# Optimization experiments

Measured on AMD Instinct MI355X. Metric: run time of the kernel, lower is better.

The kernel has to match this reference:

```python
import jax, jax.numpy as jnp
import numpy as np

B, S, D = 4, 2048, 1024

def setup_inputs() -> dict:
    key = jax.random.key(0)
    k1, k2, k3, k4 = jax.random.split(key, 4)
    scale = 1.0 / np.sqrt(D)  # roughly glorot-like magnitude for weights
    return {
        "inputs": jax.random.normal(k1, (B, S, D), dtype=jnp.float32),
        "W_query": jax.random.normal(k2, (D, D), dtype=jnp.float32) * scale,
        "W_key": jax.random.normal(k3, (D, D), dtype=jnp.float32) * scale,
        "W_value": jax.random.normal(k4, (D, D), dtype=jnp.float32) * scale,
    }

def reference(inputs, W_query, W_key, W_value):
    # QKV projections: [B,S,D] @ [D,D]
    q = jnp.einsum('bsd,de->bse', inputs, W_query)
    k = jnp.einsum('bsd,de->bse', inputs, W_key)
    v = jnp.einsum('bsd,de->bse', inputs, W_value)
    # Unscaled attention scores [B,S,S] (source applies no 1/sqrt(d))
    score = jnp.einsum('bqd,bkd->bqk', q, k)
    weights = jax.nn.softmax(score, axis=-1)
    context = jnp.einsum('bqk,bkd->bqd', weights, v)
    return context
```

## Files before the change

### kernel.cpp

```cpp
#include <hip/hip_runtime.h>
#include <math.h>


typedef __bf16 bf16;
typedef _Float16 f16;
typedef __bf16 bf16x8 __attribute__((ext_vector_type(8)));
typedef __bf16 bf16x4 __attribute__((ext_vector_type(4)));
typedef _Float16 f16x4 __attribute__((ext_vector_type(4)));
typedef _Float16 f16x8 __attribute__((ext_vector_type(8)));
typedef float  f32x4  __attribute__((ext_vector_type(4)));

template<typename E> struct vec8_of;
template<> struct vec8_of<bf16> { using type = bf16x8; };
template<> struct vec8_of<f16>  { using type = f16x8; };

__device__ inline f32x4 mfma16(bf16x8 a, bf16x8 b, f32x4 c) {
    return __builtin_amdgcn_mfma_f32_16x16x32_bf16(a, b, c, 0, 0, 0);
}
__device__ inline f32x4 mfma16(f16x8 a, f16x8 b, f32x4 c) {
    return __builtin_amdgcn_mfma_f32_16x16x32_f16(a, b, c, 0, 0, 0);
}

#define AS1 __attribute__((address_space(1)))
#define AS3 __attribute__((address_space(3)))

template<typename E>
__device__ inline void async_load16(const E* g, void* l) {
    __builtin_amdgcn_global_load_lds((const AS1 unsigned int*)g,
                                     (AS3 unsigned int*)l, 16, 0, 0);
}

#define SBAR()  do { __builtin_amdgcn_s_barrier(); __builtin_amdgcn_sched_barrier(0); } while (0)
#define WAITV(n) do { asm volatile("s_waitcnt vmcnt(" #n ")" ::: "memory"); __builtin_amdgcn_sched_barrier(0); } while (0)
#define WAITL() do { asm volatile("s_waitcnt lgkmcnt(0)" ::: "memory"); __builtin_amdgcn_sched_barrier(0); } while (0)

__device__ inline void xcd_swz(int nwg, int gx, int& bx, int& by) {
    const int flat = by * gx + bx;
    const int s = (flat & 7) * (nwg >> 3) + (flat >> 3);
    bx = s % gx;
    by = s / gx;
}

template<int OUT_MODE, int BMQ>
__device__ __forceinline__ void gemm8_body(
    char* __restrict__ smraw,
    const f16* __restrict__ A, const f16* __restrict__ B,
    float* __restrict__ Cf, f16* __restrict__ Ch,
    int K, int lda, int ldb, int ldc,
    long long sA, long long sB, long long sC,
    int bx, int by, int bz)
{
    constexpr int B0OFF = BMQ * 8192;
    constexpr int B1OFF = B0OFF + 8192;
    constexpr int BUFSZ = B0OFF + 16384;

    A += (long long)bz * sA;
    B += (long long)bz * sB;

    const int tid  = threadIdx.x;
    const int lane = tid & 63;
    const int wave = tid >> 6;
    const int quad = lane >> 4;
    const int l16  = lane & 15;
    const int wm   = wave >> 2;
    const int wn   = wave & 3;

    const long long rowA0 = (long long)by * (BMQ * 128);
    const long long colB0 = (long long)bx * 256;

    const int line0 = tid >> 3;
    const int slog  = (tid & 7) ^ (line0 & 7);
    const int aRow0 = line0 * 2 + (slog >> 2);
    const int aCol0 = (slog & 3) * 8;
    const int bRow  = ((aRow0 >> 5) << 6) + (aRow0 & 31);

    const f16* aSrc0 = A + (rowA0 + aRow0) * lda + aCol0;
    const f16* aSrc1 = A + (rowA0 + 128 + aRow0) * lda + aCol0;
    const f16* b0Src = B + (colB0 + bRow) * ldb + aCol0;
    const f16* b1Src = b0Src + 32LL * ldb;

    const int dA0 = tid * 16, dA1 = 8192 + tid * 16;

    const int nt = K >> 5;

    auto stageA = [&](int t) {
        char* buf = smraw + (t & 1) * BUFSZ;
        async_load16(aSrc0 + t * 32, buf + dA0);
        if (BMQ == 2) async_load16(aSrc1 + t * 32, buf + dA1);
    };
    auto stageB0 = [&](int t) {
        char* buf = smraw + (t & 1) * BUFSZ;
        async_load16(b0Src + t * 32, buf + B0OFF + dA0);
    };
    auto stageB1 = [&](int t) {
        char* buf = smraw + (t & 1) * BUFSZ;
        async_load16(b1Src + t * 32, buf + B1OFF + dA0);
    };

    const int h    = l16 >> 1;
    const int lofs = h * 128 + ((((l16 & 1) * 4 + quad) ^ h) << 4);
    const int aoff = wm * (BMQ * 4096) + lofs;
    const int boff = wn * 2048 + lofs;

    f32x4 acc[4 * BMQ][4];
#pragma unroll
    for (int i = 0; i < 4 * BMQ; i++)
#pragma unroll
        for (int j = 0; j < 4; j++) acc[i][j] = (f32x4){0.f, 0.f, 0.f, 0.f};

    stageA(0); stageB0(0); stageB1(0);
    stageA(1); stageB0(1);
    if constexpr (BMQ == 2) WAITV(4); else WAITV(3);
    SBAR();

    for (int t = 0; t < nt; t++) {
        const char* buf = smraw + (t & 1) * BUFSZ;
        f16x8 av[4 * BMQ], bv[2];

#pragma unroll
        for (int i = 0; i < 4 * BMQ; i++) av[i] = *(const f16x8*)(buf + aoff + i * 1024);
#pragma unroll
        for (int j = 0; j < 2; j++) bv[j] = *(const f16x8*)(buf + B0OFF + boff + j * 1024);
        if (t + 1 < nt) stageB1(t + 1);
        SBAR();
        WAITL();
        __builtin_amdgcn_s_setprio(1);
#pragma unroll
        for (int i = 0; i < 4 * BMQ; i++) {
            acc[i][0] = mfma16(av[i], bv[0], acc[i][0]);
            acc[i][1] = mfma16(av[i], bv[1], acc[i][1]);
        }
        __builtin_amdgcn_s_setprio(0);
        if (t + 1 < nt) { if constexpr (BMQ == 2) WAITV(4); else WAITV(3); }
        else WAITV(0);
        SBAR();

#pragma unroll
        for (int j = 0; j < 2; j++) bv[j] = *(const f16x8*)(buf + B1OFF + boff + j * 1024);
        if (t + 2 < nt) { stageA(t + 2); stageB0(t + 2); }
        SBAR();
        WAITL();
        __builtin_amdgcn_s_setprio(1);
#pragma unroll
        for (int i = 0; i < 4 * BMQ; i++) {
            acc[i][2] = mfma16(av[i], bv[0], acc[i][2]);
            acc[i][3] = mfma16(av[i], bv[1], acc[i][3]);
        }
        __builtin_amdgcn_s_setprio(0);
        if (t + 2 < nt) { if constexpr (BMQ == 2) WAITV(4); else WAITV(3); }
        else if (t + 1 < nt) WAITV(1);
        SBAR();
    }

    if constexpr (OUT_MODE == 2) {
        auto tr = (f16(*)[72])smraw;
        const int batch = (int)(rowA0 >> 11);
        const long long rib = rowA0 & 2047;
        const int c  = tid >> 1;
        const int r0 = (tid & 1) << 5;
#pragma unroll
        for (int h2 = 0; h2 < 2; h2++)
#pragma unroll
            for (int iq = 0; iq < 2; iq++) {
                __syncthreads();
                if (wm == h2) {
#pragma unroll
                    for (int i2 = 0; i2 < 4; i2++)
#pragma unroll
                        for (int j = 0; j < 4; j++)
#pragma unroll
                            for (int e = 0; e < 4; e++)
                                tr[wn * 64 + j * 16 + l16][i2 * 16 + quad * 4 + e] =
                                    (f16)acc[iq * 4 + i2][j][e];
                }
                __syncthreads();
                f16* vt = Ch + (long long)batch * 1024 * 2048 +
                          (long long)(colB0 + c) * ldc + rib + h2 * 128 + iq * 64 + r0;
#pragma unroll
                for (int u = 0; u < 32; u += 8)
                    *(f16x8*)(vt + u) = *(const f16x8*)&tr[c][r0 + u];
            }
        return;
    }

    const long long cOff = (long long)bz * sC +
                           (rowA0 + wm * (BMQ * 64) + quad * 4) * (long long)ldc +
                           colB0 + wn * 64 + l16;
#pragma unroll
    for (int i = 0; i < 4 * BMQ; i++)
#pragma unroll
        for (int e = 0; e < 4; e++) {
            const long long ro = cOff + (long long)(i * 16 + e) * ldc;
            if (OUT_MODE == 0) {
                float* rp = Cf + ro;
#pragma unroll
                for (int j = 0; j < 4; j++) rp[j * 16] = acc[i][j][e];
            } else {
                f16* rp = Ch + ro;
#pragma unroll
                for (int j = 0; j < 4; j++) rp[j * 16] = (f16)acc[i][j][e];
            }
        }
}

__global__ __launch_bounds__(512, 2) void tv8(
    const f16* __restrict__ Xf, const f16* __restrict__ Mt_f,
    const f16* __restrict__ Wvt_f, f16* __restrict__ T, f16* __restrict__ Vt)
{
    extern __shared__ char smraw[];
    int bx = blockIdx.x, by = blockIdx.y;
    xcd_swz(256, 8, bx, by);
    if (bx < 4)
        gemm8_body<1, 2>(smraw, Xf, Mt_f, nullptr, T, 1024, 1024, 1024, 1024,
                         0, 0, 0, bx, by, 0);
    else
        gemm8_body<2, 2>(smraw, Xf, Wvt_f, nullptr, Vt, 1024, 1024, 1024, 2048,
                         0, 0, 0, bx - 4, by, 0);
}

template<int OUT_MODE, int BMQ>
__global__ __launch_bounds__(512, 2) void gemm8_k(
    const f16* __restrict__ A, const f16* __restrict__ B,
    float* __restrict__ Cf, f16* __restrict__ Ch,
    int K, int lda, int ldb, int ldc,
    long long sA, long long sB, long long sC)
{
    extern __shared__ char smraw[];
    int bx = blockIdx.x, by = blockIdx.y;
    xcd_swz(gridDim.x * gridDim.y, gridDim.x, bx, by);
    gemm8_body<OUT_MODE, BMQ>(smraw, A, B, Cf, Ch, K, lda, ldb, ldc, sA, sB, sC,
                              bx, by, blockIdx.z);
}

template<typename E, bool SPLIT, int OUT_MODE, int BK>
__device__ __forceinline__ void gemm_body(
    char* __restrict__ smraw,
    const E* __restrict__ Ahi, const E* __restrict__ Alo,
    const E* __restrict__ Bhi, const E* __restrict__ Blo,
    float* __restrict__ Cf, f16* __restrict__ Ch,
    int K, int lda, int ldb, int ldc,
    long long sA, long long sB, long long sC,
    int bx, int by, int bz)
{
    using vec8 = typename vec8_of<E>::type;
    constexpr int TILE_BYTES = 128 * BK * (int)sizeof(E);
    constexpr int CPW = (TILE_BYTES / 1024) / 4;
    constexpr int SPR = (BK * (int)sizeof(E)) / 16;

    Ahi += (long long)bz * sA;
    Bhi += (long long)bz * sB;
    if (SPLIT) { Alo += (long long)bz * sA; Blo += (long long)bz * sB; }

    const int tid  = threadIdx.x;
    const int lane = tid & 63;
    const int wave = tid >> 6;
    const int quad = lane >> 4;
    const int l16  = lane & 15;
    const int wm   = (wave >> 1) * 64;
    const int wn   = (wave & 1) * 64;

    const long long rowA0 = (long long)by * 128;
    const long long colB0 = (long long)bx * 128;

    auto swz = [](int r) -> int { return (SPR == 8) ? (r & 7) : ((r >> 1) & 3); };

    int ofs[CPW], rr[CPW], cc8[CPW];
#pragma unroll
    for (int u = 0; u < CPW; u++) {
        ofs[u] = (wave * CPW + u) * 1024 + lane * 16;
        const int s = ofs[u] >> 4;
        rr[u]  = s / SPR;
        cc8[u] = (s & (SPR - 1)) ^ swz(rr[u]);
    }

    f32x4 acc[4][4];
#pragma unroll
    for (int i = 0; i < 4; i++)
#pragma unroll
        for (int j = 0; j < 4; j++) acc[i][j] = (f32x4){0.f, 0.f, 0.f, 0.f};

    for (int k0 = 0; k0 < K; k0 += BK) {
#pragma unroll
        for (int u = 0; u < CPW; u++) {
            async_load16(Ahi + (rowA0 + rr[u]) * lda + k0 + cc8[u] * 8, smraw + 0 * TILE_BYTES + ofs[u]);
            async_load16(Bhi + (colB0 + rr[u]) * ldb + k0 + cc8[u] * 8, smraw + 1 * TILE_BYTES + ofs[u]);
            if (SPLIT) {
                async_load16(Alo + (rowA0 + rr[u]) * lda + k0 + cc8[u] * 8, smraw + 2 * TILE_BYTES + ofs[u]);
                async_load16(Blo + (colB0 + rr[u]) * ldb + k0 + cc8[u] * 8, smraw + 3 * TILE_BYTES + ofs[u]);
            }
        }
        __syncthreads();

#pragma unroll
        for (int kh = 0; kh < BK / 32; kh++) {
            const int kc8 = kh * 4 + quad;
            vec8 a_hi[4], b_hi[4], a_lo[4], b_lo[4];
#pragma unroll
            for (int i = 0; i < 4; i++) {
                const int ra = wm + i * 16 + l16;
                const int rb = wn + i * 16 + l16;
                const int oa = ra * (SPR * 16) + ((kc8 ^ swz(ra)) << 4);
                const int ob = rb * (SPR * 16) + ((kc8 ^ swz(rb)) << 4);
                a_hi[i] = *(const vec8*)(smraw + 0 * TILE_BYTES + oa);
                b_hi[i] = *(const vec8*)(smraw + 1 * TILE_BYTES + ob);
                if (SPLIT) {
                    a_lo[i] = *(const vec8*)(smraw + 2 * TILE_BYTES + oa);
                    b_lo[i] = *(const vec8*)(smraw + 3 * TILE_BYTES + ob);
                }
            }
#pragma unroll
            for (int i = 0; i < 4; i++)
#pragma unroll
                for (int j = 0; j < 4; j++) {
                    acc[i][j] = mfma16(a_hi[i], b_hi[j], acc[i][j]);
                    if (SPLIT) {
                        acc[i][j] = mfma16(a_hi[i], b_lo[j], acc[i][j]);
                        acc[i][j] = mfma16(a_lo[i], b_hi[j], acc[i][j]);
                    }
                }
        }
        __syncthreads();
    }

    const long long cOff = (long long)bz * sC +
                           (rowA0 + wm + quad * 4) * (long long)ldc + colB0 + wn + l16;
#pragma unroll
    for (int i = 0; i < 4; i++)
#pragma unroll
        for (int e = 0; e < 4; e++) {
            const long long ro = cOff + (i * 16 + e) * ldc;
            if (OUT_MODE == 0) {
                float* rp = Cf + ro;
#pragma unroll
                for (int j = 0; j < 4; j++) rp[j * 16] = acc[i][j][e];
            } else {
                f16* rp = Ch + ro;
#pragma unroll
                for (int j = 0; j < 4; j++) rp[j * 16] = (f16)acc[i][j][e];
            }
        }
}

template<typename E, bool SPLIT, int OUT_MODE, int BK>
__global__ __launch_bounds__(256) void gemm_bt(
    const E* __restrict__ Ahi, const E* __restrict__ Alo,
    const E* __restrict__ Bhi, const E* __restrict__ Blo,
    float* __restrict__ Cf, f16* __restrict__ Ch,
    int K, int lda, int ldb, int ldc,
    long long sA, long long sB, long long sC)
{
    extern __shared__ char smraw[];
    gemm_body<E, SPLIT, OUT_MODE, BK>(smraw, Ahi, Alo, Bhi, Blo, Cf, Ch,
                                      K, lda, ldb, ldc, sA, sB, sC,
                                      blockIdx.x, blockIdx.y, blockIdx.z);
}

__global__ __launch_bounds__(256) void prep_all(
    const float4* __restrict__ X, f16* __restrict__ Xf,
    const float* __restrict__ Wq, const float* __restrict__ Wk, const float* __restrict__ Wv,
    bf16* __restrict__ Wq_h, bf16* __restrict__ Wq_l,
    bf16* __restrict__ Wk_h, bf16* __restrict__ Wk_l,
    f16* __restrict__ Wvt_f)
{
    int b = blockIdx.x;
    if (b < 8192) {
        long long i = (long long)b * 256 + threadIdx.x;
        float4 v = X[i];
        f16x4 fv = {(f16)v.x, (f16)v.y, (f16)v.z, (f16)v.w};
        *(f16x4*)(Xf + 4 * i) = fv;
    } else if (b < 10240) {
        const int b2 = b - 8192;
        const float4* W = (const float4*)(b2 < 1024 ? Wq : Wk);
        bf16* hh = b2 < 1024 ? Wq_h : Wk_h;
        bf16* ll = b2 < 1024 ? Wq_l : Wk_l;
        long long i = (long long)(b2 & 1023) * 256 + threadIdx.x;
        float4 v = W[i];
        bf16 a0 = (bf16)v.x, a1 = (bf16)v.y, a2 = (bf16)v.z, a3 = (bf16)v.w;
        bf16x4 hv = {a0, a1, a2, a3};
        bf16x4 lv = {(bf16)(v.x - (float)a0), (bf16)(v.y - (float)a1),
                     (bf16)(v.z - (float)a2), (bf16)(v.w - (float)a3)};
        *(bf16x4*)(hh + 4 * i) = hv;
        *(bf16x4*)(ll + 4 * i) = lv;
    } else {
        const int b3 = b - 10240;
        __shared__ float t[32][33];
        const int bx = (b3 & 31) * 32, by = (b3 >> 5) * 32;
        const int tx = threadIdx.x & 31, ty = threadIdx.x >> 5;
#pragma unroll
        for (int i = 0; i < 32; i += 8)
            t[ty + i][tx] = Wv[(long long)(by + ty + i) * 1024 + bx + tx];
        __syncthreads();
#pragma unroll
        for (int i = 0; i < 32; i += 8) {
            long long o = (long long)(bx + ty + i) * 1024 + by + tx;
            Wvt_f[o] = (f16)t[tx][ty + i];
        }
    }
}

__global__ __launch_bounds__(256) void softmax_f16(const float* __restrict__ S,
                                                   f16* __restrict__ P, int n)
{
    const long long row = blockIdx.x;
    const float4* p = (const float4*)(S + row * (long long)n);
    f16* q = P + row * (long long)n;
    const int tid = threadIdx.x;
    const int wv = tid >> 6, lane = tid & 63;

    float4 va = p[tid], vb = p[tid + 256];
    float v[8] = {va.x, va.y, va.z, va.w, vb.x, vb.y, vb.z, vb.w};
    float m = -3.4e38f;
#pragma unroll
    for (int i = 0; i < 8; i++) m = fmaxf(m, v[i]);
#pragma unroll
    for (int off = 32; off > 0; off >>= 1) m = fmaxf(m, __shfl_xor(m, off, 64));

    __shared__ float red[4];
    if (lane == 0) red[wv] = m;
    __syncthreads();
    m = fmaxf(fmaxf(red[0], red[1]), fmaxf(red[2], red[3]));

    float s = 0.f;
#pragma unroll
    for (int i = 0; i < 8; i++) { v[i] = __expf(v[i] - m); s += v[i]; }
#pragma unroll
    for (int off = 32; off > 0; off >>= 1) s += __shfl_xor(s, off, 64);
    __syncthreads();
    if (lane == 0) red[wv] = s;
    __syncthreads();
    s = red[0] + red[1] + red[2] + red[3];

    const float inv = 1.0f / s;
    f16x4 o0 = {(f16)(v[0] * inv), (f16)(v[1] * inv), (f16)(v[2] * inv), (f16)(v[3] * inv)};
    f16x4 o1 = {(f16)(v[4] * inv), (f16)(v[5] * inv), (f16)(v[6] * inv), (f16)(v[7] * inv)};
    *(f16x4*)(q + tid * 4) = o0;
    *(f16x4*)(q + 1024 + tid * 4) = o1;
}

extern "C" void kernel_launch(void* const* d_in, const int* in_sizes, int n_in,
                              void* d_out, int out_size, void* d_ws, size_t ws_size,
                              hipStream_t stream) {
    const float* X  = (const float*)d_in[0];
    const float* Wq = (const float*)d_in[1];
    const float* Wk = (const float*)d_in[2];
    const float* Wv = (const float*)d_in[3];
    float* out = (float*)d_out;

    char* w = (char*)d_ws;
    const long long MB = 1024LL * 1024;
    f16*  Xf    = (f16*) (w + 0 * MB);
    bf16* Wq_h  = (bf16*)(w + 16 * MB);
    bf16* Wq_l  = (bf16*)(w + 18 * MB);
    bf16* Wk_h  = (bf16*)(w + 20 * MB);
    bf16* Wk_l  = (bf16*)(w + 22 * MB);
    f16*  Wvt_f = (f16*) (w + 24 * MB);
    f16*  Mt_f  = (f16*) (w + 26 * MB);
    f16*  T     = (f16*) (w + 28 * MB);
    f16*  Vt    = (f16*) (w + 44 * MB);
    float* Sc   = (float*)(w + 60 * MB);
    f16*  P     = (f16*) (w + 124 * MB);

    dim3 blk(256);

    prep_all<<<dim3(11264), blk, 0, stream>>>(
        (const float4*)X, Xf, Wq, Wk, Wv, Wq_h, Wq_l, Wk_h, Wk_l, Wvt_f);

    gemm_bt<bf16, true, 1, 32><<<dim3(8, 8, 1), blk, 32768, stream>>>(
        Wk_h, Wk_l, Wq_h, Wq_l, nullptr, Mt_f,
        1024, 1024, 1024, 1024, 0, 0, 0);

    tv8<<<dim3(8, 32), dim3(512), 65536, stream>>>(Xf, Mt_f, Wvt_f, T, Vt);

    gemm8_k<0, 2><<<dim3(8, 8, 4), dim3(512), 65536, stream>>>(
        T, Xf, Sc, nullptr, 1024, 1024, 1024, 2048,
        2048LL * 1024, 2048LL * 1024, 2048LL * 2048);

    softmax_f16<<<dim3(4 * 2048), blk, 0, stream>>>(Sc, P, 2048);

    gemm8_k<0, 1><<<dim3(4, 16, 4), dim3(512), 49152, stream>>>(
        P, Vt, out, nullptr, 2048, 2048, 2048, 1024,
        2048LL * 2048, 1024LL * 2048, 2048LL * 1024);
}
```

Baseline: 273.3 us.

## Add deep-K double-buffered GEMM variant with 64-wide K stages for main GEMMs

Adds a new GEMM body that stages 64 K-elements per iteration (two 32-wide halves) into double-buffered LDS, splitting A and B loads across sub-phases so global loads overlap the MFMA work. Launches use 128KB/96KB of dynamic shared memory, with a fallback to the old kernels if the attribute cannot be set. It targets fewer barriers and loop iterations per K and better latency hiding, at the cost of LDS capacity and possibly fewer resident blocks per CU.

```diff
diff --git a/kernel.cpp b/kernel.cpp
--- a/kernel.cpp
+++ b/kernel.cpp
@@ -39,6 +39,220 @@
     const int s = (flat & 7) * (nwg >> 3) + (flat >> 3);
     bx = s % gx;
     by = s / gx;
+}
+
+template<int OUT_MODE, int BMQ>
+__device__ __forceinline__ void gemm_deep_body(
+    char* __restrict__ smraw,
+    const f16* __restrict__ A, const f16* __restrict__ B,
+    float* __restrict__ Cf, f16* __restrict__ Ch,
+    int K, int lda, int ldb, int ldc,
+    long long sA, long long sB, long long sC,
+    int bx, int by, int bz)
+{
+    constexpr int ACH   = BMQ * 8192;
+    constexpr int BOFF  = 2 * ACH;
+    constexpr int BUFSZ = 2 * ACH + 32768;
+    constexpr int nI    = 4 * BMQ;
+
+    A += (long long)bz * sA;
+    B += (long long)bz * sB;
+
+    const int tid  = threadIdx.x;
+    const int lane = tid & 63;
+    const int wave = tid >> 6;
+    const int quad = lane >> 4;
+    const int l16  = lane & 15;
+    const int wm   = wave >> 2;
+    const int wn   = wave & 3;
+
+    const long long rowA0 = (long long)by * (BMQ * 128);
+    const long long colB0 = (long long)bx * 256;
+
+    const int line0 = tid >> 3;
+    const int slog  = (tid & 7) ^ (line0 & 7);
+    const int r0s   = line0 * 2 + (slog >> 2);
+    const int c0s   = (slog & 3) * 8;
+
+    const f16* aSrc0 = A + (rowA0 + r0s) * lda + c0s;
+    const f16* aSrc1 = A + (rowA0 + 128 + r0s) * lda + c0s;
+    const f16* bSrc0 = B + (colB0 + r0s) * ldb + c0s;
+    const f16* bSrc1 = B + (colB0 + 128 + r0s) * ldb + c0s;
+
+    const int nt = K >> 6;
+
+    auto stageA = [&](int t, int kh) {
+        char* dst = smraw + (t & 1) * BUFSZ + kh * ACH;
+        const int k0 = t * 64 + kh * 32;
+        async_load16(aSrc0 + k0, dst + tid * 16);
+        if constexpr (BMQ == 2) async_load16(aSrc1 + k0, dst + 8192 + tid * 16);
+    };
+    auto stageB = [&](int t, int kh) {
+        char* dst = smraw + (t & 1) * BUFSZ + BOFF + kh * 16384;
+        const int k0 = t * 64 + kh * 32;
+        async_load16(bSrc0 + k0, dst + tid * 16);
+        async_load16(bSrc1 + k0, dst + 8192 + tid * 16);
+    };
+
+    const int h    = l16 >> 1;
+    const int lofs = h * 128 + ((((l16 & 1) * 4 + quad) ^ h) << 4);
+    const int aoff = wm * (ACH / 2) + lofs;
+    const int boff = BOFF + wn * 4096 + lofs;
+
+    f32x4 acc[nI][4];
+#pragma unroll
+    for (int i = 0; i < nI; i++)
+#pragma unroll
+        for (int j = 0; j < 4; j++) acc[i][j] = (f32x4){0.f, 0.f, 0.f, 0.f};
+
+    stageA(0, 0); stageA(0, 1); stageB(0, 0); stageB(0, 1);
+    WAITV(2);
+    SBAR();
+
+    for (int t = 0; t < nt; t++) {
+        const char* buf = smraw + (t & 1) * BUFSZ;
+        f16x8 av[nI], bv[2];
+
+#pragma unroll
+        for (int i = 0; i < nI; i++) av[i] = *(const f16x8*)(buf + aoff + i * 1024);
+        bv[0] = *(const f16x8*)(buf + boff);
+        bv[1] = *(const f16x8*)(buf + boff + 1024);
+        if (t + 1 < nt) { stageA(t + 1, 0); stageA(t + 1, 1); }
+        SBAR();
+        WAITL();
+        __builtin_amdgcn_s_setprio(1);
+#pragma unroll
+        for (int i = 0; i < nI; i++) {
+            acc[i][0] = mfma16(av[i], bv[0], acc[i][0]);
+            acc[i][1] = mfma16(av[i], bv[1], acc[i][1]);
+        }
+        __builtin_amdgcn_s_setprio(0);
+        SBAR();
+
+        bv[0] = *(const f16x8*)(buf + boff + 2048);
+        bv[1] = *(const f16x8*)(buf + boff + 3072);
+        if (t + 1 < nt) { stageB(t + 1, 0); stageB(t + 1, 1); }
+        SBAR();
+        WAITL();
+        __builtin_amdgcn_s_setprio(1);
+#pragma unroll
+        for (int i = 0; i < nI; i++) {
+            acc[i][2] = mfma16(av[i], bv[0], acc[i][2]);
+            acc[i][3] = mfma16(av[i], bv[1], acc[i][3]);
+        }
+        __builtin_amdgcn_s_setprio(0);
+        if (t + 1 < nt) { if constexpr (BMQ == 2) WAITV(8); else WAITV(6); }
+        else { WAITV(0); }
+        SBAR();
+
+#pragma unroll
+        for (int i = 0; i < nI; i++) av[i] = *(const f16x8*)(buf + ACH + aoff + i * 1024);
+        bv[0] = *(const f16x8*)(buf + 16384 + boff);
+        bv[1] = *(const f16x8*)(buf + 16384 + boff + 1024);
+        SBAR();
+        WAITL();
+        __builtin_amdgcn_s_setprio(1);
+#pragma unroll
+        for (int i = 0; i < nI; i++) {
+            acc[i][0] = mfma16(av[i], bv[0], acc[i][0]);
+            acc[i][1] = mfma16(av[i], bv[1], acc[i][1]);
+        }
+        __builtin_amdgcn_s_setprio(0);
+        SBAR();
+
+        bv[0] = *(const f16x8*)(buf + 16384 + boff + 2048);
+        bv[1] = *(const f16x8*)(buf + 16384 + boff + 3072);
+        SBAR();
+        WAITL();
+        __builtin_amdgcn_s_setprio(1);
+#pragma unroll
+        for (int i = 0; i < nI; i++) {
+            acc[i][2] = mfma16(av[i], bv[0], acc[i][2]);
+            acc[i][3] = mfma16(av[i], bv[1], acc[i][3]);
+        }
+        __builtin_amdgcn_s_setprio(0);
+        if (t + 1 < nt) { WAITV(2); } else { WAITV(0); }
+        SBAR();
+    }
+
+    if constexpr (OUT_MODE == 2) {
+        auto tr = (f16(*)[72])smraw;
+        const int batch = (int)(rowA0 >> 11);
+        const long long rib = rowA0 & 2047;
+        const int c  = tid >> 1;
+        const int r0 = (tid & 1) << 5;
+#pragma unroll
+        for (int h2 = 0; h2 < 2; h2++)
+#pragma unroll
+            for (int iq = 0; iq < 2; iq++) {
+                __syncthreads();
+                if (wm == h2) {
+#pragma unroll
+                    for (int i2 = 0; i2 < 4; i2++)
+#pragma unroll
+                        for (int j = 0; j < 4; j++)
+#pragma unroll
+                            for (int e = 0; e < 4; e++)
+                                tr[wn * 64 + j * 16 + l16][i2 * 16 + quad * 4 + e] =
+                                    (f16)acc[iq * 4 + i2][j][e];
+                }
+                __syncthreads();
+                f16* vt = Ch + (long long)batch * 1024 * 2048 +
+                          (long long)(colB0 + c) * ldc + rib + h2 * 128 + iq * 64 + r0;
+#pragma unroll
+                for (int u = 0; u < 32; u += 8)
+                    *(f16x8*)(vt + u) = *(const f16x8*)&tr[c][r0 + u];
+            }
+        return;
+    }
+
+    const long long cOff = (long long)bz * sC +
+                           (rowA0 + wm * (BMQ * 64) + quad * 4) * (long long)ldc +
+                           colB0 + wn * 64 + l16;
+#pragma unroll
+    for (int i = 0; i < nI; i++)
+#pragma unroll
+        for (int e = 0; e < 4; e++) {
+            const long long ro = cOff + (long long)(i * 16 + e) * ldc;
+            if (OUT_MODE == 0) {
+                float* rp = Cf + ro;
+#pragma unroll
+                for (int j = 0; j < 4; j++) rp[j * 16] = acc[i][j][e];
+            } else {
+                f16* rp = Ch + ro;
+#pragma unroll
+                for (int j = 0; j < 4; j++) rp[j * 16] = (f16)acc[i][j][e];
+            }
+        }
+}
+
+__global__ __launch_bounds__(512, 2) void tv8d(
+    const f16* __restrict__ Xf, const f16* __restrict__ Mt_f,
+    const f16* __restrict__ Wvt_f, f16* __restrict__ T, f16* __restrict__ Vt)
+{
+    extern __shared__ char smraw[];
+    int bx = blockIdx.x, by = blockIdx.y;
+    xcd_swz(256, 8, bx, by);
+    if (bx < 4)
+        gemm_deep_body<1, 2>(smraw, Xf, Mt_f, nullptr, T, 1024, 1024, 1024, 1024,
+                             0, 0, 0, bx, by, 0);
+    else
+        gemm_deep_body<2, 2>(smraw, Xf, Wvt_f, nullptr, Vt, 1024, 1024, 1024, 2048,
+                             0, 0, 0, bx - 4, by, 0);
+}
+
+template<int OUT_MODE, int BMQ>
+__global__ __launch_bounds__(512, 2) void gemmd_k(
+    const f16* __restrict__ A, const f16* __restrict__ B,
+    float* __restrict__ Cf, f16* __restrict__ Ch,
+    int K, int lda, int ldb, int ldc,
+    long long sA, long long sB, long long sC)
+{
+    extern __shared__ char smraw[];
+    int bx = blockIdx.x, by = blockIdx.y;
+    xcd_swz(gridDim.x * gridDim.y, gridDim.x, bx, by);
+    gemm_deep_body<OUT_MODE, BMQ>(smraw, A, B, Cf, Ch, K, lda, ldb, ldc,
+                                  sA, sB, sC, bx, by, blockIdx.z);
 }
 
 template<int OUT_MODE, int BMQ>
@@ -460,6 +674,22 @@
     float* Sc   = (float*)(w + 60 * MB);
     f16*  P     = (f16*) (w + 124 * MB);
 
+    static int deep_ok = -1;
+    if (deep_ok < 0) {
+        auto* pSc = gemmd_k<0, 2>;
+        auto* pPv = gemmd_k<0, 1>;
+        hipError_t e1 = hipFuncSetAttribute(
+            reinterpret_cast<const void*>(tv8d),
+            hipFuncAttributeMaxDynamicSharedMemorySize, 131072);
+        hipError_t e2 = hipFuncSetAttribute(
+            reinterpret_cast<const void*>(pSc),
+            hipFuncAttributeMaxDynamicSharedMemorySize, 131072);
+        hipError_t e3 = hipFuncSetAttribute(
+            reinterpret_cast<const void*>(pPv),
+            hipFuncAttributeMaxDynamicSharedMemorySize, 98304);
+        deep_ok = (e1 == hipSuccess && e2 == hipSuccess && e3 == hipSuccess) ? 1 : 0;
+    }
+
     dim3 blk(256);
 
     prep_all<<<dim3(11264), blk, 0, stream>>>(
@@ -469,15 +699,23 @@
         Wk_h, Wk_l, Wq_h, Wq_l, nullptr, Mt_f,
         1024, 1024, 1024, 1024, 0, 0, 0);
 
-    tv8<<<dim3(8, 32), dim3(512), 65536, stream>>>(Xf, Mt_f, Wvt_f, T, Vt);
-
-    gemm8_k<0, 2><<<dim3(8, 8, 4), dim3(512), 65536, stream>>>(
-        T, Xf, Sc, nullptr, 1024, 1024, 1024, 2048,
-        2048LL * 1024, 2048LL * 1024, 2048LL * 2048);
-
-    softmax_f16<<<dim3(4 * 2048), blk, 0, stream>>>(Sc, P, 2048);
-
-    gemm8_k<0, 1><<<dim3(4, 16, 4), dim3(512), 49152, stream>>>(
-        P, Vt, out, nullptr, 2048, 2048, 2048, 1024,
-        2048LL * 2048, 1024LL * 2048, 2048LL * 1024);
-}
+    if (deep_ok) {
+        tv8d<<<dim3(8, 32), dim3(512), 131072, stream>>>(Xf, Mt_f, Wvt_f, T, Vt);
+        gemmd_k<0, 2><<<dim3(8, 8, 4), dim3(512), 131072, stream>>>(
+            T, Xf, Sc, nullptr, 1024, 1024, 1024, 2048,
+            2048LL * 1024, 2048LL * 1024, 2048LL * 2048);
+        softmax_f16<<<dim3(4 * 2048), blk, 0, stream>>>(Sc, P, 2048);
+        gemmd_k<0, 1><<<dim3(4, 16, 4), dim3(512), 98304, stream>>>(
+            P, Vt, out, nullptr, 2048, 2048, 2048, 1024,
+            2048LL * 2048, 1024LL * 2048, 2048LL * 1024);
+    } else {
+        tv8<<<dim3(8, 32), dim3(512), 65536, stream>>>(Xf, Mt_f, Wvt_f, T, Vt);
+        gemm8_k<0, 2><<<dim3(8, 8, 4), dim3(512), 65536, stream>>>(
+            T, Xf, Sc, nullptr, 1024, 1024, 1024, 2048,
+            2048LL * 1024, 2048LL * 1024, 2048LL * 2048);
+        softmax_f16<<<dim3(4 * 2048), blk, 0, stream>>>(Sc, P, 2048);
+        gemm8_k<0, 1><<<dim3(4, 16, 4), dim3(512), 49152, stream>>>(
+            P, Vt, out, nullptr, 2048, 2048, 2048, 1024,
+            2048LL * 2048, 1024LL * 2048, 2048LL * 1024);
+    }
+}
```

After: 275.2 us. No clear change (+0.7%).

## Replace 8-wave GEMMs with deep-K pipelined projection kernel and simpler batched GEMMs

Applied to the files above, without the earlier changes.

Replaces the 8-wave gemm8 kernels with a K=64-per-stage double-buffered projection kernel (tv8d) that uses 128KB of LDS. A fallback double-buffered 256-thread kernel is used if that attribute cannot be set. The score GEMM and the P·V GEMM move to the generic single-buffered 128x128 gemm_body path. That path is simpler but loses the tuned 8-wave ping-pong pipeline on the two largest GEMMs, so it risks lower MFMA utilization and less overlap.

```diff
diff --git a/kernel.cpp b/kernel.cpp
--- a/kernel.cpp
+++ b/kernel.cpp
@@ -41,198 +41,7 @@
     by = s / gx;
 }
 
-template<int OUT_MODE, int BMQ>
-__device__ __forceinline__ void gemm8_body(
-    char* __restrict__ smraw,
-    const f16* __restrict__ A, const f16* __restrict__ B,
-    float* __restrict__ Cf, f16* __restrict__ Ch,
-    int K, int lda, int ldb, int ldc,
-    long long sA, long long sB, long long sC,
-    int bx, int by, int bz)
-{
-    constexpr int B0OFF = BMQ * 8192;
-    constexpr int B1OFF = B0OFF + 8192;
-    constexpr int BUFSZ = B0OFF + 16384;
-
-    A += (long long)bz * sA;
-    B += (long long)bz * sB;
-
-    const int tid  = threadIdx.x;
-    const int lane = tid & 63;
-    const int wave = tid >> 6;
-    const int quad = lane >> 4;
-    const int l16  = lane & 15;
-    const int wm   = wave >> 2;
-    const int wn   = wave & 3;
-
-    const long long rowA0 = (long long)by * (BMQ * 128);
-    const long long colB0 = (long long)bx * 256;
-
-    const int line0 = tid >> 3;
-    const int slog  = (tid & 7) ^ (line0 & 7);
-    const int aRow0 = line0 * 2 + (slog >> 2);
-    const int aCol0 = (slog & 3) * 8;
-    const int bRow  = ((aRow0 >> 5) << 6) + (aRow0 & 31);
-
-    const f16* aSrc0 = A + (rowA0 + aRow0) * lda + aCol0;
-    const f16* aSrc1 = A + (rowA0 + 128 + aRow0) * lda + aCol0;
-    const f16* b0Src = B + (colB0 + bRow) * ldb + aCol0;
-    const f16* b1Src = b0Src + 32LL * ldb;
-
-    const int dA0 = tid * 16, dA1 = 8192 + tid * 16;
-
-    const int nt = K >> 5;
-
-    auto stageA = [&](int t) {
-        char* buf = smraw + (t & 1) * BUFSZ;
-        async_load16(aSrc0 + t * 32, buf + dA0);
-        if (BMQ == 2) async_load16(aSrc1 + t * 32, buf + dA1);
-    };
-    auto stageB0 = [&](int t) {
-        char* buf = smraw + (t & 1) * BUFSZ;
-        async_load16(b0Src + t * 32, buf + B0OFF + dA0);
-    };
-    auto stageB1 = [&](int t) {
-        char* buf = smraw + (t & 1) * BUFSZ;
-        async_load16(b1Src + t * 32, buf + B1OFF + dA0);
-    };
-
-    const int h    = l16 >> 1;
-    const int lofs = h * 128 + ((((l16 & 1) * 4 + quad) ^ h) << 4);
-    const int aoff = wm * (BMQ * 4096) + lofs;
-    const int boff = wn * 2048 + lofs;
-
-    f32x4 acc[4 * BMQ][4];
-#pragma unroll
-    for (int i = 0; i < 4 * BMQ; i++)
-#pragma unroll
-        for (int j = 0; j < 4; j++) acc[i][j] = (f32x4){0.f, 0.f, 0.f, 0.f};
-
-    stageA(0); stageB0(0); stageB1(0);
-    stageA(1); stageB0(1);
-    if constexpr (BMQ == 2) WAITV(4); else WAITV(3);
-    SBAR();
-
-    for (int t = 0; t < nt; t++) {
-        const char* buf = smraw + (t & 1) * BUFSZ;
-        f16x8 av[4 * BMQ], bv[2];
-
-#pragma unroll
-        for (int i = 0; i < 4 * BMQ; i++) av[i] = *(const f16x8*)(buf + aoff + i * 1024);
-#pragma unroll
-        for (int j = 0; j < 2; j++) bv[j] = *(const f16x8*)(buf + B0OFF + boff + j * 1024);
-        if (t + 1 < nt) stageB1(t + 1);
-        SBAR();
-        WAITL();
-        __builtin_amdgcn_s_setprio(1);
-#pragma unroll
-        for (int i = 0; i < 4 * BMQ; i++) {
-            acc[i][0] = mfma16(av[i], bv[0], acc[i][0]);
-            acc[i][1] = mfma16(av[i], bv[1], acc[i][1]);
-        }
-        __builtin_amdgcn_s_setprio(0);
-        if (t + 1 < nt) { if constexpr (BMQ == 2) WAITV(4); else WAITV(3); }
-        else WAITV(0);
-        SBAR();
-
-#pragma unroll
-        for (int j = 0; j < 2; j++) bv[j] = *(const f16x8*)(buf + B1OFF + boff + j * 1024);
-        if (t + 2 < nt) { stageA(t + 2); stageB0(t + 2); }
-        SBAR();
-        WAITL();
-        __builtin_amdgcn_s_setprio(1);
-#pragma unroll
-        for (int i = 0; i < 4 * BMQ; i++) {
-            acc[i][2] = mfma16(av[i], bv[0], acc[i][2]);
-            acc[i][3] = mfma16(av[i], bv[1], acc[i][3]);
-        }
-        __builtin_amdgcn_s_setprio(0);
-        if (t + 2 < nt) { if constexpr (BMQ == 2) WAITV(4); else WAITV(3); }
-        else if (t + 1 < nt) WAITV(1);
-        SBAR();
-    }
-
-    if constexpr (OUT_MODE == 2) {
-        auto tr = (f16(*)[72])smraw;
-        const int batch = (int)(rowA0 >> 11);
-        const long long rib = rowA0 & 2047;
-        const int c  = tid >> 1;
-        const int r0 = (tid & 1) << 5;
-#pragma unroll
-        for (int h2 = 0; h2 < 2; h2++)
-#pragma unroll
-            for (int iq = 0; iq < 2; iq++) {
-                __syncthreads();
-                if (wm == h2) {
-#pragma unroll
-                    for (int i2 = 0; i2 < 4; i2++)
-#pragma unroll
-                        for (int j = 0; j < 4; j++)
-#pragma unroll
-                            for (int e = 0; e < 4; e++)
-                                tr[wn * 64 + j * 16 + l16][i2 * 16 + quad * 4 + e] =
-                                    (f16)acc[iq * 4 + i2][j][e];
-                }
-                __syncthreads();
-                f16* vt = Ch + (long long)batch * 1024 * 2048 +
-                          (long long)(colB0 + c) * ldc + rib + h2 * 128 + iq * 64 + r0;
-#pragma unroll
-                for (int u = 0; u < 32; u += 8)
-                    *(f16x8*)(vt + u) = *(const f16x8*)&tr[c][r0 + u];
-            }
-        return;
-    }
-
-    const long long cOff = (long long)bz * sC +
-                           (rowA0 + wm * (BMQ * 64) + quad * 4) * (long long)ldc +
-                           colB0 + wn * 64 + l16;
-#pragma unroll
-    for (int i = 0; i < 4 * BMQ; i++)
-#pragma unroll
-        for (int e = 0; e < 4; e++) {
-            const long long ro = cOff + (long long)(i * 16 + e) * ldc;
-            if (OUT_MODE == 0) {
-                float* rp = Cf + ro;
-#pragma unroll
-                for (int j = 0; j < 4; j++) rp[j * 16] = acc[i][j][e];
-            } else {
-                f16* rp = Ch + ro;
-#pragma unroll
-                for (int j = 0; j < 4; j++) rp[j * 16] = (f16)acc[i][j][e];
-            }
-        }
-}
-
-__global__ __launch_bounds__(512, 2) void tv8(
-    const f16* __restrict__ Xf, const f16* __restrict__ Mt_f,
-    const f16* __restrict__ Wvt_f, f16* __restrict__ T, f16* __restrict__ Vt)
-{
-    extern __shared__ char smraw[];
-    int bx = blockIdx.x, by = blockIdx.y;
-    xcd_swz(256, 8, bx, by);
-    if (bx < 4)
-        gemm8_body<1, 2>(smraw, Xf, Mt_f, nullptr, T, 1024, 1024, 1024, 1024,
-                         0, 0, 0, bx, by, 0);
-    else
-        gemm8_body<2, 2>(smraw, Xf, Wvt_f, nullptr, Vt, 1024, 1024, 1024, 2048,
-                         0, 0, 0, bx - 4, by, 0);
-}
-
-template<int OUT_MODE, int BMQ>
-__global__ __launch_bounds__(512, 2) void gemm8_k(
-    const f16* __restrict__ A, const f16* __restrict__ B,
-    float* __restrict__ Cf, f16* __restrict__ Ch,
-    int K, int lda, int ldb, int ldc,
-    long long sA, long long sB, long long sC)
-{
-    extern __shared__ char smraw[];
-    int bx = blockIdx.x, by = blockIdx.y;
-    xcd_swz(gridDim.x * gridDim.y, gridDim.x, bx, by);
-    gemm8_body<OUT_MODE, BMQ>(smraw, A, B, Cf, Ch, K, lda, ldb, ldc, sA, sB, sC,
-                              bx, by, blockIdx.z);
-}
-
-template<typename E, bool SPLIT, int OUT_MODE, int BK>
+template<typename E, bool SPLIT, int OUT_MODE, int BK, bool DBUF>
 __device__ __forceinline__ void gemm_body(
     char* __restrict__ smraw,
     const E* __restrict__ Ahi, const E* __restrict__ Alo,
@@ -246,6 +55,7 @@
     constexpr int TILE_BYTES = 128 * BK * (int)sizeof(E);
     constexpr int CPW = (TILE_BYTES / 1024) / 4;
     constexpr int SPR = (BK * (int)sizeof(E)) / 16;
+    constexpr int NMAT = SPLIT ? 4 : 2;
 
     Ahi += (long long)bz * sA;
     Bhi += (long long)bz * sB;
@@ -279,18 +89,21 @@
 #pragma unroll
         for (int j = 0; j < 4; j++) acc[i][j] = (f32x4){0.f, 0.f, 0.f, 0.f};
 
-    for (int k0 = 0; k0 < K; k0 += BK) {
+    auto stage = [&](int k0, int buf) {
+        char* base = smraw + buf * (NMAT * TILE_BYTES);
 #pragma unroll
         for (int u = 0; u < CPW; u++) {
-            async_load16(Ahi + (rowA0 + rr[u]) * lda + k0 + cc8[u] * 8, smraw + 0 * TILE_BYTES + ofs[u]);
-            async_load16(Bhi + (colB0 + rr[u]) * ldb + k0 + cc8[u] * 8, smraw + 1 * TILE_BYTES + ofs[u]);
+            async_load16(Ahi + (rowA0 + rr[u]) * lda + k0 + cc8[u] * 8, base + 0 * TILE_BYTES + ofs[u]);
+            async_load16(Bhi + (colB0 + rr[u]) * ldb + k0 + cc8[u] * 8, base + 1 * TILE_BYTES + ofs[u]);
             if (SPLIT) {
-                async_load16(Alo + (rowA0 + rr[u]) * lda + k0 + cc8[u] * 8, smraw + 2 * TILE_BYTES + ofs[u]);
-                async_load16(Blo + (colB0 + rr[u]) * ldb + k0 + cc8[u] * 8, smraw + 3 * TILE_BYTES + ofs[u]);
+                async_load16(Alo + (rowA0 + rr[u]) * lda + k0 + cc8[u] * 8, base + 2 * TILE_BYTES + ofs[u]);
+                async_load16(Blo + (colB0 + rr[u]) * ldb + k0 + cc8[u] * 8, base + 3 * TILE_BYTES + ofs[u]);
             }
         }
-        __syncthreads();
-
+    };
+
+    auto compute = [&](int buf) {
+        char* base = smraw + buf * (NMAT * TILE_BYTES);
 #pragma unroll
         for (int kh = 0; kh < BK / 32; kh++) {
             const int kc8 = kh * 4 + quad;
@@ -301,11 +114,11 @@
                 const int rb = wn + i * 16 + l16;
                 const int oa = ra * (SPR * 16) + ((kc8 ^ swz(ra)) << 4);
                 const int ob = rb * (SPR * 16) + ((kc8 ^ swz(rb)) << 4);
-                a_hi[i] = *(const vec8*)(smraw + 0 * TILE_BYTES + oa);
-                b_hi[i] = *(const vec8*)(smraw + 1 * TILE_BYTES + ob);
+                a_hi[i] = *(const vec8*)(base + 0 * TILE_BYTES + oa);
+                b_hi[i] = *(const vec8*)(base + 1 * TILE_BYTES + ob);
                 if (SPLIT) {
-                    a_lo[i] = *(const vec8*)(smraw + 2 * TILE_BYTES + oa);
-                    b_lo[i] = *(const vec8*)(smraw + 3 * TILE_BYTES + ob);
+                    a_lo[i] = *(const vec8*)(base + 2 * TILE_BYTES + oa);
+                    b_lo[i] = *(const vec8*)(base + 3 * TILE_BYTES + ob);
                 }
             }
 #pragma unroll
@@ -319,7 +132,55 @@
                     }
                 }
         }
+    };
+
+    if (DBUF) {
+        const int nt = K / BK;
+        stage(0, 0);
+        for (int t = 0; t < nt; t++) {
+            const int cur = t & 1;
+            if (t + 1 < nt) {
+                stage((t + 1) * BK, cur ^ 1);
+                asm volatile("s_waitcnt vmcnt(4)" ::: "memory");
+            } else {
+                asm volatile("s_waitcnt vmcnt(0)" ::: "memory");
+            }
+            __builtin_amdgcn_s_barrier();
+            asm volatile("" ::: "memory");
+            compute(cur);
+            asm volatile("s_waitcnt lgkmcnt(0)" ::: "memory");
+            __builtin_amdgcn_sched_barrier(0);
+            __builtin_amdgcn_s_barrier();
+            asm volatile("" ::: "memory");
+        }
+    } else {
+        for (int k0 = 0; k0 < K; k0 += BK) {
+            stage(k0, 0);
+            __syncthreads();
+            compute(0);
+            __syncthreads();
+        }
+    }
+
+    if (OUT_MODE == 2) {
+        auto tr = (f16(*)[130])smraw;
+#pragma unroll
+        for (int i = 0; i < 4; i++)
+#pragma unroll
+            for (int j = 0; j < 4; j++)
+#pragma unroll
+                for (int e = 0; e < 4; e++)
+                    tr[wn + j * 16 + l16][wm + i * 16 + quad * 4 + e] = (f16)acc[i][j][e];
         __syncthreads();
+        const int batch = (int)(rowA0 >> 11);
+        const int rib   = (int)(rowA0 & 2047);
+        const int c  = tid >> 1;
+        const int r0 = (tid & 1) << 6;
+        f16* vt = Ch + (long long)batch * 1024 * 2048 + (long long)(colB0 + c) * ldc + rib + r0;
+#pragma unroll
+        for (int u = 0; u < 64; u += 8)
+            *(f16x8*)(vt + u) = *(const f16x8*)&tr[c][r0 + u];
+        return;
     }
 
     const long long cOff = (long long)bz * sC +
@@ -339,6 +200,21 @@
                 for (int j = 0; j < 4; j++) rp[j * 16] = (f16)acc[i][j][e];
             }
         }
+}
+
+template<int OUT_MODE>
+__global__ __launch_bounds__(256) void gemm_lt(
+    const f16* __restrict__ A, const f16* __restrict__ B,
+    float* __restrict__ Cf, f16* __restrict__ Ch,
+    int K, int lda, int ldb, int ldc,
+    long long sA, long long sB, long long sC)
+{
+    extern __shared__ char smraw[];
+    int bx = blockIdx.x, by = blockIdx.y;
+    xcd_swz(gridDim.x * gridDim.y, gridDim.x, bx, by);
+    gemm_body<f16, false, OUT_MODE, 32, false>(smraw, A, nullptr, B, nullptr,
+                                               Cf, Ch, K, lda, ldb, ldc,
+                                               sA, sB, sC, bx, by, blockIdx.z);
 }
 
 template<typename E, bool SPLIT, int OUT_MODE, int BK>
@@ -350,9 +226,225 @@
     long long sA, long long sB, long long sC)
 {
     extern __shared__ char smraw[];
-    gemm_body<E, SPLIT, OUT_MODE, BK>(smraw, Ahi, Alo, Bhi, Blo, Cf, Ch,
-                                      K, lda, ldb, ldc, sA, sB, sC,
-                                      blockIdx.x, blockIdx.y, blockIdx.z);
+    gemm_body<E, SPLIT, OUT_MODE, BK, false>(smraw, Ahi, Alo, Bhi, Blo, Cf, Ch,
+                                             K, lda, ldb, ldc, sA, sB, sC,
+                                             blockIdx.x, blockIdx.y, blockIdx.z);
+}
+
+__global__ __launch_bounds__(256) void tv_gemm(
+    const f16* __restrict__ Xf, const f16* __restrict__ Mt_f,
+    const f16* __restrict__ Wvt_f,
+    f16* __restrict__ T, f16* __restrict__ Vt)
+{
+    extern __shared__ char smraw[];
+    if (blockIdx.x < 8)
+        gemm_body<f16, false, 1, 32, true>(smraw, Xf, nullptr, Mt_f, nullptr,
+                                           nullptr, T, 1024, 1024, 1024, 1024,
+                                           0, 0, 0, blockIdx.x, blockIdx.y, 0);
+    else
+        gemm_body<f16, false, 2, 32, true>(smraw, Xf, nullptr, Wvt_f, nullptr,
+                                           nullptr, Vt, 1024, 1024, 1024, 2048,
+                                           0, 0, 0, blockIdx.x - 8, blockIdx.y, 0);
+}
+
+template<int OUT_MODE, int BMQ>
+__device__ __forceinline__ void gemm_deep_body(
+    char* __restrict__ smraw,
+    const f16* __restrict__ A, const f16* __restrict__ B,
+    float* __restrict__ Cf, f16* __restrict__ Ch,
+    int K, int lda, int ldb, int ldc,
+    long long sA, long long sB, long long sC,
+    int bx, int by, int bz)
+{
+    constexpr int ACH   = BMQ * 8192;
+    constexpr int BOFF  = 2 * ACH;
+    constexpr int BUFSZ = 2 * ACH + 32768;
+    constexpr int nI    = 4 * BMQ;
+
+    A += (long long)bz * sA;
+    B += (long long)bz * sB;
+
+    const int tid  = threadIdx.x;
+    const int lane = tid & 63;
+    const int wave = tid >> 6;
+    const int quad = lane >> 4;
+    const int l16  = lane & 15;
+    const int wm   = wave >> 2;
+    const int wn   = wave & 3;
+
+    const long long rowA0 = (long long)by * (BMQ * 128);
+    const long long colB0 = (long long)bx * 256;
+
+    const int line0 = tid >> 3;
+    const int slog  = (tid & 7) ^ (line0 & 7);
+    const int r0s   = line0 * 2 + (slog >> 2);
+    const int c0s   = (slog & 3) * 8;
+
+    const f16* aSrc0 = A + (rowA0 + r0s) * lda + c0s;
+    const f16* aSrc1 = A + (rowA0 + 128 + r0s) * lda + c0s;
+    const f16* bSrc0 = B + (colB0 + r0s) * ldb + c0s;
+    const f16* bSrc1 = B + (colB0 + 128 + r0s) * ldb + c0s;
+
+    const int nt = K >> 6;
+
+    auto stageA = [&](int t, int kh) {
+        char* dst = smraw + (t & 1) * BUFSZ + kh * ACH;
+        const int k0 = t * 64 + kh * 32;
+        async_load16(aSrc0 + k0, dst + tid * 16);
+        if constexpr (BMQ == 2) async_load16(aSrc1 + k0, dst + 8192 + tid * 16);
+    };
+    auto stageB = [&](int t, int kh) {
+        char* dst = smraw + (t & 1) * BUFSZ + BOFF + kh * 16384;
+        const int k0 = t * 64 + kh * 32;
+        async_load16(bSrc0 + k0, dst + tid * 16);
+        async_load16(bSrc1 + k0, dst + 8192 + tid * 16);
+    };
+
+    const int h    = l16 >> 1;
+    const int lofs = h * 128 + ((((l16 & 1) * 4 + quad) ^ h) << 4);
+    const int aoff = wm * (ACH / 2) + lofs;
+    const int boff = BOFF + wn * 4096 + lofs;
+
+    f32x4 acc[nI][4];
+#pragma unroll
+    for (int i = 0; i < nI; i++)
+#pragma unroll
+        for (int j = 0; j < 4; j++) acc[i][j] = (f32x4){0.f, 0.f, 0.f, 0.f};
+
+    stageA(0, 0); stageA(0, 1); stageB(0, 0); stageB(0, 1);
+    WAITV(2);
+    SBAR();
+
+    for (int t = 0; t < nt; t++) {
+        const char* buf = smraw + (t & 1) * BUFSZ;
+        f16x8 av[nI], bv[2];
+
+#pragma unroll
+        for (int i = 0; i < nI; i++) av[i] = *(const f16x8*)(buf + aoff + i * 1024);
+        bv[0] = *(const f16x8*)(buf + boff);
+        bv[1] = *(const f16x8*)(buf + boff + 1024);
+        if (t + 1 < nt) { stageA(t + 1, 0); stageA(t + 1, 1); }
+        SBAR();
+        WAITL();
+        __builtin_amdgcn_s_setprio(1);
+#pragma unroll
+        for (int i = 0; i < nI; i++) {
+            acc[i][0] = mfma16(av[i], bv[0], acc[i][0]);
+            acc[i][1] = mfma16(av[i], bv[1], acc[i][1]);
+        }
+        __builtin_amdgcn_s_setprio(0);
+        SBAR();
+
+        bv[0] = *(const f16x8*)(buf + boff + 2048);
+        bv[1] = *(const f16x8*)(buf + boff + 3072);
+        if (t + 1 < nt) { stageB(t + 1, 0); stageB(t + 1, 1); }
+        SBAR();
+        WAITL();
+        __builtin_amdgcn_s_setprio(1);
+#pragma unroll
+        for (int i = 0; i < nI; i++) {
+            acc[i][2] = mfma16(av[i], bv[0], acc[i][2]);
+            acc[i][3] = mfma16(av[i], bv[1], acc[i][3]);
+        }
+        __builtin_amdgcn_s_setprio(0);
+        if (t + 1 < nt) { if constexpr (BMQ == 2) WAITV(8); else WAITV(6); }
+        else { WAITV(0); }
+        SBAR();
+
+#pragma unroll
+        for (int i = 0; i < nI; i++) av[i] = *(const f16x8*)(buf + ACH + aoff + i * 1024);
+        bv[0] = *(const f16x8*)(buf + 16384 + boff);
+        bv[1] = *(const f16x8*)(buf + 16384 + boff + 1024);
+        SBAR();
+        WAITL();
+        __builtin_amdgcn_s_setprio(1);
+#pragma unroll
+        for (int i = 0; i < nI; i++) {
+            acc[i][0] = mfma16(av[i], bv[0], acc[i][0]);
+            acc[i][1] = mfma16(av[i], bv[1], acc[i][1]);
+        }
+        __builtin_amdgcn_s_setprio(0);
+        SBAR();
+
+        bv[0] = *(const f16x8*)(buf + 16384 + boff + 2048);
+        bv[1] = *(const f16x8*)(buf + 16384 + boff + 3072);
+        SBAR();
+        WAITL();
+        __builtin_amdgcn_s_setprio(1);
+#pragma unroll
+        for (int i = 0; i < nI; i++) {
+            acc[i][2] = mfma16(av[i], bv[0], acc[i][2]);
+            acc[i][3] = mfma16(av[i], bv[1], acc[i][3]);
+        }
+        __builtin_amdgcn_s_setprio(0);
+        if (t + 1 < nt) { WAITV(2); } else { WAITV(0); }
+        SBAR();
+    }
+
+    if constexpr (OUT_MODE == 2) {
+        auto tr = (f16(*)[72])smraw;
+        const int batch = (int)(rowA0 >> 11);
+        const long long rib = rowA0 & 2047;
+        const int c  = tid >> 1;
+        const int r0 = (tid & 1) << 5;
+#pragma unroll
+        for (int h2 = 0; h2 < 2; h2++)
+#pragma unroll
+            for (int iq = 0; iq < 2; iq++) {
+                __syncthreads();
+                if (wm == h2) {
+#pragma unroll
+                    for (int i2 = 0; i2 < 4; i2++)
+#pragma unroll
+                        for (int j = 0; j < 4; j++)
+#pragma unroll
+                            for (int e = 0; e < 4; e++)
+                                tr[wn * 64 + j * 16 + l16][i2 * 16 + quad * 4 + e] =
+                                    (f16)acc[iq * 4 + i2][j][e];
+                }
+                __syncthreads();
+                f16* vt = Ch + (long long)batch * 1024 * 2048 +
+                          (long long)(colB0 + c) * ldc + rib + h2 * 128 + iq * 64 + r0;
+#pragma unroll
+                for (int u = 0; u < 32; u += 8)
+                    *(f16x8*)(vt + u) = *(const f16x8*)&tr[c][r0 + u];
+            }
+        return;
+    }
+
+    const long long cOff = (long long)bz * sC +
+                           (rowA0 + wm * (BMQ * 64) + quad * 4) * (long long)ldc +
+                           colB0 + wn * 64 + l16;
+#pragma unroll
+    for (int i = 0; i < nI; i++)
+#pragma unroll
+        for (int e = 0; e < 4; e++) {
+            const long long ro = cOff + (long long)(i * 16 + e) * ldc;
+            if (OUT_MODE == 0) {
+                float* rp = Cf + ro;
+#pragma unroll
+                for (int j = 0; j < 4; j++) rp[j * 16] = acc[i][j][e];
+            } else {
+                f16* rp = Ch + ro;
+#pragma unroll
+                for (int j = 0; j < 4; j++) rp[j * 16] = (f16)acc[i][j][e];
+            }
+        }
+}
+
+__global__ __launch_bounds__(512, 2) void tv8d(
+    const f16* __restrict__ Xf, const f16* __restrict__ Mt_f,
+    const f16* __restrict__ Wvt_f, f16* __restrict__ T, f16* __restrict__ Vt)
+{
+    extern __shared__ char smraw[];
+    int bx = blockIdx.x, by = blockIdx.y;
+    xcd_swz(256, 8, bx, by);
+    if (bx < 4)
+        gemm_deep_body<1, 2>(smraw, Xf, Mt_f, nullptr, T, 1024, 1024, 1024, 1024,
+                             0, 0, 0, bx, by, 0);
+    else
+        gemm_deep_body<2, 2>(smraw, Xf, Wvt_f, nullptr, Vt, 1024, 1024, 1024, 2048,
+                             0, 0, 0, bx - 4, by, 0);
 }
 
 __global__ __launch_bounds__(256) void prep_all(
@@ -460,6 +552,14 @@
     float* Sc   = (float*)(w + 60 * MB);
     f16*  P     = (f16*) (w + 124 * MB);
 
+    static int deep_ok = -1;
+    if (deep_ok < 0) {
+        hipError_t e1 = hipFuncSetAttribute(
+            reinterpret_cast<const void*>(tv8d),
+            hipFuncAttributeMaxDynamicSharedMemorySize, 131072);
+        deep_ok = (e1 == hipSuccess) ? 1 : 0;
+    }
+
     dim3 blk(256);
 
     prep_all<<<dim3(11264), blk, 0, stream>>>(
@@ -469,15 +569,18 @@
         Wk_h, Wk_l, Wq_h, Wq_l, nullptr, Mt_f,
         1024, 1024, 1024, 1024, 0, 0, 0);
 
-    tv8<<<dim3(8, 32), dim3(512), 65536, stream>>>(Xf, Mt_f, Wvt_f, T, Vt);
-
-    gemm8_k<0, 2><<<dim3(8, 8, 4), dim3(512), 65536, stream>>>(
+    if (deep_ok)
+        tv8d<<<dim3(8, 32), dim3(512), 131072, stream>>>(Xf, Mt_f, Wvt_f, T, Vt);
+    else
+        tv_gemm<<<dim3(16, 64), blk, 33280, stream>>>(Xf, Mt_f, Wvt_f, T, Vt);
+
+    gemm_lt<0><<<dim3(16, 16, 4), blk, 16384, stream>>>(
         T, Xf, Sc, nullptr, 1024, 1024, 1024, 2048,
         2048LL * 1024, 2048LL * 1024, 2048LL * 2048);
 
     softmax_f16<<<dim3(4 * 2048), blk, 0, stream>>>(Sc, P, 2048);
 
-    gemm8_k<0, 1><<<dim3(4, 16, 4), dim3(512), 49152, stream>>>(
+    gemm_lt<0><<<dim3(8, 16, 4), blk, 16384, stream>>>(
         P, Vt, out, nullptr, 2048, 2048, 2048, 1024,
         2048LL * 2048, 1024LL * 2048, 2048LL * 1024);
 }
```

New measurement: 310.4 us. 1.14x slower.
